# Kernel optimization log

Measured on AMD Instinct MI355X. Metric: run time of the kernel, lower is better.

The kernel has to match this reference:

```python
import jax, jax.numpy as jnp
import numpy as np

N = 50000      # nodes
E = 600000     # edges
D = 128        # num_features == hidden_dim
H = 1          # heads (only runnable config of this module)
C = 128        # per-head channels
L = 2          # num_layers
G = 64         # graphs in batch
NC = 10        # num_classes


def setup_inputs() -> dict:
    key = jax.random.key(0)
    ks = jax.random.split(key, 12)
    s = 1.0 / np.sqrt(D)
    inp = {
        "x": jax.random.normal(ks[0], (N, D), jnp.float32),
        "edge_index": jax.random.randint(ks[1], (2, E), 0, N),
        "batch": jnp.sort(jax.random.randint(ks[2], (N,), 0, G)),
        # per-layer TransformerConv params (stacked over layers)
        "Wq": jax.random.normal(ks[3], (L, D, H * C), jnp.float32) * s,
        "bq": jax.random.normal(ks[4], (L, H * C), jnp.float32) * 0.01,
        "Wk": jax.random.normal(ks[5], (L, D, H * C), jnp.float32) * s,
        "bk": jax.random.normal(ks[6], (L, H * C), jnp.float32) * 0.01,
        "Wv": jax.random.normal(ks[7], (L, D, H * C), jnp.float32) * s,
        "bv": jax.random.normal(ks[8], (L, H * C), jnp.float32) * 0.01,
        "Ws": jax.random.normal(ks[9], (L, D, H * C), jnp.float32) * s,  # lin_skip (root weight)
        "bs": jax.random.normal(ks[10], (L, H * C), jnp.float32) * 0.01,
        "W_fc": jax.random.normal(ks[11], (H * C, NC), jnp.float32) * (1.0 / np.sqrt(H * C)),
        "b_fc": jnp.zeros((NC,), jnp.float32),
    }
    return inp


def _transformer_conv(x, src, dst, wq, bq, wk, bk, wv, bv, ws, bs):
    n = x.shape[0]
    q = (x @ wq + bq).reshape(n, H, C)
    k = (x @ wk + bk).reshape(n, H, C)
    v = (x @ wv + bv).reshape(n, H, C)
    # edge-wise gather: query from dst (x_i), key/value from src (x_j)
    score = (q[dst] * k[src]).sum(-1) / jnp.sqrt(jnp.float32(C))  # [E, H]
    # segment softmax over incoming edges of each dst node
    m = jax.ops.segment_max(score, dst, num_segments=n)           # [N, H]
    ex = jnp.exp(score - m[dst])
    den = jax.ops.segment_sum(ex, dst, num_segments=n)
    alpha = ex / den[dst]                                         # [E, H]
    agg = jax.ops.segment_sum(alpha[..., None] * v[src], dst, num_segments=n)
    return agg.reshape(n, H * C) + x @ ws + bs                    # concat heads + skip


def reference(x, edge_index, batch, Wq, bq, Wk, bk, Wv, bv, Ws, bs, W_fc, b_fc):
    src, dst = edge_index[0], edge_index[1]
    h = x
    for l in range(L):
        h = jax.nn.relu(_transformer_conv(h, src, dst, Wq[l], bq[l], Wk[l], bk[l],
                                          Wv[l], bv[l], Ws[l], bs[l]))
    # global mean pool per graph
    sums = jax.ops.segment_sum(h, batch, num_segments=G)
    cnts = jax.ops.segment_sum(jnp.ones((h.shape[0],), h.dtype), batch, num_segments=G)
    pooled = sums / jnp.maximum(cnts, 1.0)[:, None]
    logits = pooled @ W_fc + b_fc
    return jax.nn.log_softmax(logits, axis=1)
```

## Files before the change

### kernel.cpp

```cpp
#include <hip/hip_runtime.h>
#include <math.h>

#define NN 50000
#define EE 600000
#define DD 128
#define GG 64
#define NCLS 10
#define PCHUNK 128
#define NTILE (NN / 16)
#define NBUK 196
#define BSTRIDE 4096
#define EPB ((EE + 255) / 256)

typedef __attribute__((ext_vector_type(8))) __bf16 bf16x8;
typedef __attribute__((ext_vector_type(8))) unsigned short u16x8;
typedef __attribute__((ext_vector_type(4))) float f32x4;

__device__ __forceinline__ unsigned short f2bf(float f) {
    unsigned int u = __float_as_uint(f);
    u += 0x7fff + ((u >> 16) & 1);
    return (unsigned short)(u >> 16);
}

__device__ __forceinline__ float bf2f(unsigned short h) {
    return __uint_as_float(((unsigned int)h) << 16);
}


__global__ __launch_bounds__(256) void prep_kernel(
    const float* __restrict__ x,
    const float* __restrict__ wq, const float* __restrict__ wk,
    const float* __restrict__ wv, const float* __restrict__ ws,
    unsigned short* __restrict__ wt, unsigned short* __restrict__ xb,
    int* __restrict__ bucketcnt, float* __restrict__ gsum) {
    int tid = blockIdx.x * 256 + threadIdx.x;
    int TOT = gridDim.x * 256;
    if (tid < 256) bucketcnt[tid] = 0;
    for (int i = tid; i < GG * DD + GG; i += TOT) gsum[i] = 0.f;
    for (int i = tid; i < 2 * 4 * 16384; i += TOT) {
        int k = i & 127;
        int n = (i >> 7) & 127;
        int lm = i >> 14;
        int l = lm >> 2, m = lm & 3;
        const float* w = (m == 0) ? wq : (m == 1) ? wk : (m == 2) ? wv : ws;
        wt[i] = f2bf(w[l * 16384 + k * 128 + n]);
    }
    const int NV = (int)(((size_t)NN * DD) / 8);
    for (int i = tid; i < NV; i += TOT) {
        const float* p = x + (size_t)i * 8;
        float4 f0 = *(const float4*)p;
        float4 f1 = *(const float4*)(p + 4);
        u16x8 a8;
        a8[0] = f2bf(f0.x); a8[1] = f2bf(f0.y); a8[2] = f2bf(f0.z); a8[3] = f2bf(f0.w);
        a8[4] = f2bf(f1.x); a8[5] = f2bf(f1.y); a8[6] = f2bf(f1.z); a8[7] = f2bf(f1.w);
        *(u16x8*)(xb + (size_t)i * 8) = a8;
    }
}


__global__ __launch_bounds__(1024) void bucket_kernel(
    const int* __restrict__ src, const int* __restrict__ dst,
    int* __restrict__ bucketcnt, int2* __restrict__ bedge) {
    __shared__ int hist[256];
    __shared__ int base[256];
    int t = threadIdx.x;
    if (t < 256) hist[t] = 0;
    __syncthreads();
    int e0 = blockIdx.x * EPB;
    int eend = min(e0 + EPB, EE);

    int b0 = -1, b1 = -1, b2 = -1;
    int sl0 = 0, sl1 = 0, sl2 = 0;
    int s0 = 0, s1 = 0, s2 = 0, d0 = 0, d1 = 0, d2 = 0;
    int i = e0 + t;
    if (i < eend) { d0 = dst[i]; s0 = src[i]; b0 = d0 >> 8; sl0 = atomicAdd(&hist[b0], 1); }
    i += 1024;
    if (i < eend) { d1 = dst[i]; s1 = src[i]; b1 = d1 >> 8; sl1 = atomicAdd(&hist[b1], 1); }
    i += 1024;
    if (i < eend) { d2 = dst[i]; s2 = src[i]; b2 = d2 >> 8; sl2 = atomicAdd(&hist[b2], 1); }
    __syncthreads();

    if (t < 256) {
        int h = hist[t];
        base[t] = h ? atomicAdd(&bucketcnt[t], h) : 0;
    }
    __syncthreads();

    if (b0 >= 0) bedge[b0 * BSTRIDE + base[b0] + sl0] = make_int2(s0, d0);
    if (b1 >= 0) bedge[b1 * BSTRIDE + base[b1] + sl1] = make_int2(s1, d1);
    if (b2 >= 0) bedge[b2 * BSTRIDE + base[b2] + sl2] = make_int2(s2, d2);
}


__global__ __launch_bounds__(1024) void bsort_kernel(
    const int* __restrict__ bucketcnt, const int2* __restrict__ bedge,
    int* __restrict__ indptr, int* __restrict__ esrc) {
    __shared__ int buf[256];
    __shared__ int cur[256];
    __shared__ int bstart_s;
    int b = blockIdx.x;
    int t = threadIdx.x;

    if (t < 256) buf[t] = (t < NBUK) ? bucketcnt[t] : 0;
    __syncthreads();
    if (t == 0) {
        int acc = 0;
        for (int i2 = 0; i2 < NBUK; ++i2) {
            if (i2 == b) bstart_s = acc;
            acc += buf[i2];
        }
    }
    if (b == 0 && t == 1) indptr[NN] = EE;
    __syncthreads();

    int count = buf[b];
    int node0 = b << 8;
    int nn = min(256, NN - node0);
    __syncthreads();
    if (t < 256) buf[t] = 0;
    __syncthreads();

    const int2* be = bedge + (size_t)b * BSTRIDE;
    for (int i2 = t; i2 < count; i2 += 1024)
        atomicAdd(&buf[be[i2].y - node0], 1);
    __syncthreads();

    if (t == 0) {
        int acc = 0;
        for (int i2 = 0; i2 < 256; ++i2) {
            cur[i2] = acc;
            acc += buf[i2];
        }
    }
    __syncthreads();
    if (t < nn) indptr[node0 + t] = bstart_s + cur[t];
    __syncthreads();

    for (int i2 = t; i2 < count; i2 += 1024) {
        int2 e = be[i2];
        int slot = atomicAdd(&cur[e.y - node0], 1);
        esrc[bstart_s + slot] = e.x;
    }
}


__global__ __launch_bounds__(256, 4) void gemm_mfma(
    const unsigned short* __restrict__ xa,
    const unsigned short* __restrict__ wt,
    const float* __restrict__ bq, const float* __restrict__ bk,
    const float* __restrict__ bv, const float* __restrict__ bs,
    unsigned short* __restrict__ qb, unsigned short* __restrict__ kvb,
    unsigned short* __restrict__ sb) {
    int gw = blockIdx.x * 4 + (threadIdx.x >> 6);
    int lane = threadIdx.x & 63;
    int mat = (gw >> 1) & 3;
    int ch = gw & 1;
    int wseq = gw >> 3;
    int lr = lane & 15, quad = lane >> 4;

    const unsigned short* wm_ = wt + mat * 16384;
    const float* bias = (mat == 0) ? bq : (mat == 1) ? bk : (mat == 2) ? bv : bs;
    unsigned short* outp; int ostride, ooff;
    if (mat == 0)      { outp = qb;  ostride = 128; ooff = 0; }
    else if (mat == 1) { outp = kvb; ostride = 256; ooff = 0; }
    else if (mat == 2) { outp = kvb; ostride = 256; ooff = 128; }
    else               { outp = sb;  ostride = 128; ooff = 0; }

    bf16x8 bfr[4][4];
    #pragma unroll
    for (int ks = 0; ks < 4; ++ks)
        #pragma unroll
        for (int tn = 0; tn < 4; ++tn)
            bfr[ks][tn] = *(const bf16x8*)(wm_ + (ch * 64 + tn * 16 + lr) * 128
                                               + ks * 32 + quad * 8);
    float bcol[4];
    #pragma unroll
    for (int tn = 0; tn < 4; ++tn) bcol[tn] = bias[ch * 64 + tn * 16 + lr];

    for (int tile = wseq; tile < NTILE; tile += 256) {
        int row0 = tile * 16;
        bf16x8 af[4];
        #pragma unroll
        for (int ks = 0; ks < 4; ++ks)
            af[ks] = *(const bf16x8*)(xa + (size_t)(row0 + lr) * DD + ks * 32 + quad * 8);

        f32x4 acc[4];
        #pragma unroll
        for (int tn = 0; tn < 4; ++tn) acc[tn] = (f32x4){0.f, 0.f, 0.f, 0.f};
        #pragma unroll
        for (int ks = 0; ks < 4; ++ks)
            #pragma unroll
            for (int tn = 0; tn < 4; ++tn)
                acc[tn] = __builtin_amdgcn_mfma_f32_16x16x32_bf16(
                    af[ks], bfr[ks][tn], acc[tn], 0, 0, 0);

        #pragma unroll
        for (int tn = 0; tn < 4; ++tn) {
            int col = ch * 64 + tn * 16 + lr;
            int nb = row0 + quad * 4;
            #pragma unroll
            for (int r = 0; r < 4; ++r)
                outp[(size_t)(nb + r) * ostride + ooff + col] = f2bf(acc[tn][r] + bcol[tn]);
        }
    }
}


__global__ __launch_bounds__(256) void attn_kernel(
    const unsigned short* __restrict__ qb, const unsigned short* __restrict__ kvb,
    const unsigned short* __restrict__ sb,
    const int* __restrict__ indptr, const int* __restrict__ esrc,
    unsigned short* __restrict__ hout, int n) {
    int node = (int)((blockIdx.x * blockDim.x + threadIdx.x) >> 6);
    int lane = threadIdx.x & 63;
    if (node >= n) return;
    int g = lane >> 4, j = lane & 15;

    u16x8 q8 = *(const u16x8*)(qb + (size_t)node * DD + j * 8);
    float qf[8];
    #pragma unroll
    for (int c = 0; c < 8; ++c) qf[c] = bf2f(q8[c]);

    int beg = indptr[node], end = indptr[node + 1];

    float m = -3.0e38f, den = 0.f;
    float acc[8];
    #pragma unroll
    for (int c = 0; c < 8; ++c) acc[c] = 0.f;

    int e = beg + g;
    if (e < end) {
        const unsigned short* p0 = kvb + (size_t)esrc[e] * 256 + j * 8;
        u16x8 k8 = *(const u16x8*)p0;
        u16x8 v8 = *(const u16x8*)(p0 + 128);
        for (;;) {
            int en = e + 4;
            bool haven = en < end;
            u16x8 k8n, v8n;
            if (haven) {
                const unsigned short* p = kvb + (size_t)esrc[en] * 256 + j * 8;
                k8n = *(const u16x8*)p;
                v8n = *(const u16x8*)(p + 128);
            }
            float p_;
            p_ = qf[0] * bf2f(k8[0]);
            p_ = fmaf(qf[1], bf2f(k8[1]), p_);
            p_ = fmaf(qf[2], bf2f(k8[2]), p_);
            p_ = fmaf(qf[3], bf2f(k8[3]), p_);
            p_ = fmaf(qf[4], bf2f(k8[4]), p_);
            p_ = fmaf(qf[5], bf2f(k8[5]), p_);
            p_ = fmaf(qf[6], bf2f(k8[6]), p_);
            p_ = fmaf(qf[7], bf2f(k8[7]), p_);
            p_ += __shfl_xor(p_, 8);
            p_ += __shfl_xor(p_, 4);
            p_ += __shfl_xor(p_, 2);
            p_ += __shfl_xor(p_, 1);
            float score = p_ * 0.088388347648318447f;
            float mn = fmaxf(m, score);
            float scale = __expf(m - mn);
            float pe = __expf(score - mn);
            den = den * scale + pe;
            #pragma unroll
            for (int c = 0; c < 8; ++c)
                acc[c] = fmaf(acc[c], scale, pe * bf2f(v8[c]));
            m = mn;
            if (!haven) break;
            e = en; k8 = k8n; v8 = v8n;
        }
    }

    float mo = __shfl_xor(m, 16);
    float m2 = fmaxf(m, mo);
    mo = __shfl_xor(m2, 32);
    float mf = fmaxf(m2, mo);
    float sc = __expf(m - mf);
    den *= sc;
    den += __shfl_xor(den, 16);
    den += __shfl_xor(den, 32);
    #pragma unroll
    for (int c = 0; c < 8; ++c) {
        float a = acc[c] * sc;
        a += __shfl_xor(a, 16);
        a += __shfl_xor(a, 32);
        acc[c] = a;
    }
    float inv = den > 0.f ? 1.0f / den : 0.f;
    if (g == 0) {
        u16x8 s8 = *(const u16x8*)(sb + (size_t)node * DD + j * 8);
        u16x8 o8;
        #pragma unroll
        for (int c = 0; c < 8; ++c)
            o8[c] = f2bf(fmaxf(fmaf(acc[c], inv, bf2f(s8[c])), 0.f));
        *(u16x8*)(hout + (size_t)node * DD + j * 8) = o8;
    }
}


__global__ __launch_bounds__(128) void pool_kernel(const unsigned short* __restrict__ h,
                                                   const int* __restrict__ batch,
                                                   float* __restrict__ gsum,
                                                   float* __restrict__ gcnt, int n) {
    __shared__ int bsh[PCHUNK];
    int t = threadIdx.x;
    int node0 = blockIdx.x * PCHUNK;
    int nnodes = min(PCHUNK, n - node0);
    if (t < nnodes) bsh[t] = batch[node0 + t];
    __syncthreads();

    int cur = bsh[0];
    float acc = 0.f;
    int cnt = 0;
    for (int j = 0; j < nnodes; ++j) {
        int g = bsh[j];
        float val = bf2f(h[(size_t)(node0 + j) * DD + t]);
        if (g != cur) {
            atomicAdd(&gsum[cur * DD + t], acc);
            if (t == 0) atomicAdd(&gcnt[cur], (float)cnt);
            acc = 0.f; cnt = 0; cur = g;
        }
        acc += val; ++cnt;
    }
    if (cnt > 0) {
        atomicAdd(&gsum[cur * DD + t], acc);
        if (t == 0) atomicAdd(&gcnt[cur], (float)cnt);
    }
}


__global__ __launch_bounds__(64) void head_kernel(
    const float* __restrict__ gsum, const float* __restrict__ gcnt,
    const float* __restrict__ wfc, const float* __restrict__ bfc,
    float* __restrict__ out) {
    int g = blockIdx.x;
    int lane = threadIdx.x;
    float cnt = fmaxf(gcnt[g], 1.0f);
    float inv = 1.0f / cnt;
    float p0 = gsum[g * DD + lane] * inv;
    float p1 = gsum[g * DD + lane + 64] * inv;
    __shared__ float logits[NCLS];
    for (int c = 0; c < NCLS; ++c) {
        float partial = p0 * wfc[lane * NCLS + c] + p1 * wfc[(lane + 64) * NCLS + c];
        partial += __shfl_xor(partial, 32);
        partial += __shfl_xor(partial, 16);
        partial += __shfl_xor(partial, 8);
        partial += __shfl_xor(partial, 4);
        partial += __shfl_xor(partial, 2);
        partial += __shfl_xor(partial, 1);
        if (lane == 0) logits[c] = partial + bfc[c];
    }
    __syncthreads();
    if (lane == 0) {
        float mx = logits[0];
        for (int c = 1; c < NCLS; ++c) mx = fmaxf(mx, logits[c]);
        float sum = 0.f;
        for (int c = 0; c < NCLS; ++c) sum += expf(logits[c] - mx);
        float lse = mx + logf(sum);
        for (int c = 0; c < NCLS; ++c) out[g * NCLS + c] = logits[c] - lse;
    }
}


extern "C" void kernel_launch(void* const* d_in, const int* in_sizes, int n_in,
                              void* d_out, int out_size, void* d_ws, size_t ws_size,
                              hipStream_t stream) {
    const float* x     = (const float*)d_in[0];
    const int*   ei    = (const int*)d_in[1];
    const int*   batch = (const int*)d_in[2];
    const float* Wq = (const float*)d_in[3];
    const float* bq = (const float*)d_in[4];
    const float* Wk = (const float*)d_in[5];
    const float* bk = (const float*)d_in[6];
    const float* Wv = (const float*)d_in[7];
    const float* bv = (const float*)d_in[8];
    const float* Ws = (const float*)d_in[9];
    const float* bs = (const float*)d_in[10];
    const float* Wfc = (const float*)d_in[11];
    const float* bfc = (const float*)d_in[12];
    float* out = (float*)d_out;

    const size_t ND = (size_t)NN * DD;
    unsigned short* hbuf = (unsigned short*)d_ws;
    unsigned short* qb  = hbuf + ND;
    unsigned short* sb  = qb + ND;
    unsigned short* kvb = sb + ND;
    unsigned short* xb  = kvb + 2 * ND;
    unsigned short* wt  = xb + ND;
    int* bucketcnt = (int*)(wt + 2 * 4 * 16384);
    int* indptr    = bucketcnt + 256;
    int* esrc      = indptr + NN + 1;
    int2* bedge    = (int2*)(esrc + EE);
    float* gsum = (float*)(bedge + NBUK * BSTRIDE);
    float* gcnt = gsum + GG * DD;

    const int* src = ei;
    const int* dst = ei + EE;

    prep_kernel<<<1024, 256, 0, stream>>>(x, Wq, Wk, Wv, Ws, wt, xb, bucketcnt, gsum);
    bucket_kernel<<<256, 1024, 0, stream>>>(src, dst, bucketcnt, bedge);
    bsort_kernel<<<NBUK, 1024, 0, stream>>>(bucketcnt, bedge, indptr, esrc);

    for (int l = 0; l < 2; ++l) {
        size_t bo = (size_t)l * DD;
        const unsigned short* wtl = wt + (size_t)l * 4 * 16384;
        const unsigned short* xa = (l == 0) ? xb : hbuf;
        gemm_mfma<<<512, 256, 0, stream>>>(
            xa, wtl, bq + bo, bk + bo, bv + bo, bs + bo, qb, kvb, sb);
        attn_kernel<<<(NN + 3) / 4, 256, 0, stream>>>(
            qb, kvb, sb, indptr, esrc, hbuf, NN);
    }

    pool_kernel<<<(NN + PCHUNK - 1) / PCHUNK, 128, 0, stream>>>(hbuf, batch, gsum, gcnt, NN);
    head_kernel<<<GG, 64, 0, stream>>>(gsum, gcnt, Wfc, bfc, out);
}
```

Before: 285.5 us.

## Fuse x bf16 conversion into layer-0 GEMM, parallelize bsort scans, prefetch esrc

Removes the separate fp32-to-bf16 conversion of x from prep_kernel and converts x on the fly inside a templated layer-0 GEMM, which drops a full write and re-read of a bf16 copy of x. The serial single-thread prefix sums in bsort_kernel become wave-level shuffle scans. The attention loop also loads edge source indices two steps ahead so the index load is off the critical path of the K/V gather. The cost is that layer-0 GEMM reads fp32 input, so each of the 8 waves covering a row tile reloads and reconverts the same rows at double the bytes.

```diff
diff --git a/kernel.cpp b/kernel.cpp
--- a/kernel.cpp
+++ b/kernel.cpp
@@ -28,10 +28,9 @@
 
 
 __global__ __launch_bounds__(256) void prep_kernel(
-    const float* __restrict__ x,
     const float* __restrict__ wq, const float* __restrict__ wk,
     const float* __restrict__ wv, const float* __restrict__ ws,
-    unsigned short* __restrict__ wt, unsigned short* __restrict__ xb,
+    unsigned short* __restrict__ wt,
     int* __restrict__ bucketcnt, float* __restrict__ gsum) {
     int tid = blockIdx.x * 256 + threadIdx.x;
     int TOT = gridDim.x * 256;
@@ -45,16 +44,6 @@
         const float* w = (m == 0) ? wq : (m == 1) ? wk : (m == 2) ? wv : ws;
         wt[i] = f2bf(w[l * 16384 + k * 128 + n]);
     }
-    const int NV = (int)(((size_t)NN * DD) / 8);
-    for (int i = tid; i < NV; i += TOT) {
-        const float* p = x + (size_t)i * 8;
-        float4 f0 = *(const float4*)p;
-        float4 f1 = *(const float4*)(p + 4);
-        u16x8 a8;
-        a8[0] = f2bf(f0.x); a8[1] = f2bf(f0.y); a8[2] = f2bf(f0.z); a8[3] = f2bf(f0.w);
-        a8[4] = f2bf(f1.x); a8[5] = f2bf(f1.y); a8[6] = f2bf(f1.z); a8[7] = f2bf(f1.w);
-        *(u16x8*)(xb + (size_t)i * 8) = a8;
-    }
 }
 
 
@@ -97,25 +86,32 @@
     int* __restrict__ indptr, int* __restrict__ esrc) {
     __shared__ int buf[256];
     __shared__ int cur[256];
-    __shared__ int bstart_s;
     int b = blockIdx.x;
     int t = threadIdx.x;
 
     if (t < 256) buf[t] = (t < NBUK) ? bucketcnt[t] : 0;
     __syncthreads();
-    if (t == 0) {
-        int acc = 0;
-        for (int i2 = 0; i2 < NBUK; ++i2) {
-            if (i2 == b) bstart_s = acc;
-            acc += buf[i2];
-        }
-    }
-    if (b == 0 && t == 1) indptr[NN] = EE;
-    __syncthreads();
-
+    if (t < 64) {
+        int carry = 0;
+        #pragma unroll
+        for (int c = 0; c < 4; ++c) {
+            int v = buf[c * 64 + t];
+            int x = v;
+            #pragma unroll
+            for (int off = 1; off < 64; off <<= 1) {
+                int y = __shfl_up(x, off);
+                if (t >= off) x += y;
+            }
+            cur[c * 64 + t] = carry + x - v;
+            carry += __shfl(x, 63);
+        }
+    }
+    __syncthreads();
     int count = buf[b];
+    int bstart = cur[b];
     int node0 = b << 8;
     int nn = min(256, NN - node0);
+    if (b == 0 && t == 0) indptr[NN] = EE;
     __syncthreads();
     if (t < 256) buf[t] = 0;
     __syncthreads();
@@ -125,27 +121,36 @@
         atomicAdd(&buf[be[i2].y - node0], 1);
     __syncthreads();
 
-    if (t == 0) {
-        int acc = 0;
-        for (int i2 = 0; i2 < 256; ++i2) {
-            cur[i2] = acc;
-            acc += buf[i2];
-        }
-    }
-    __syncthreads();
-    if (t < nn) indptr[node0 + t] = bstart_s + cur[t];
+    if (t < 64) {
+        int carry = 0;
+        #pragma unroll
+        for (int c = 0; c < 4; ++c) {
+            int v = buf[c * 64 + t];
+            int x = v;
+            #pragma unroll
+            for (int off = 1; off < 64; off <<= 1) {
+                int y = __shfl_up(x, off);
+                if (t >= off) x += y;
+            }
+            cur[c * 64 + t] = carry + x - v;
+            carry += __shfl(x, 63);
+        }
+    }
+    __syncthreads();
+    if (t < nn) indptr[node0 + t] = bstart + cur[t];
     __syncthreads();
 
     for (int i2 = t; i2 < count; i2 += 1024) {
         int2 e = be[i2];
         int slot = atomicAdd(&cur[e.y - node0], 1);
-        esrc[bstart_s + slot] = e.x;
-    }
-}
-
-
+        esrc[bstart + slot] = e.x;
+    }
+}
+
+
+template <bool IN_BF16>
 __global__ __launch_bounds__(256, 4) void gemm_mfma(
-    const unsigned short* __restrict__ xa,
+    const void* __restrict__ xin,
     const unsigned short* __restrict__ wt,
     const float* __restrict__ bq, const float* __restrict__ bk,
     const float* __restrict__ bv, const float* __restrict__ bs,
@@ -181,8 +186,21 @@
         int row0 = tile * 16;
         bf16x8 af[4];
         #pragma unroll
-        for (int ks = 0; ks < 4; ++ks)
-            af[ks] = *(const bf16x8*)(xa + (size_t)(row0 + lr) * DD + ks * 32 + quad * 8);
+        for (int ks = 0; ks < 4; ++ks) {
+            if (IN_BF16) {
+                af[ks] = *(const bf16x8*)((const unsigned short*)xin
+                             + (size_t)(row0 + lr) * DD + ks * 32 + quad * 8);
+            } else {
+                const float* p = (const float*)xin
+                                 + (size_t)(row0 + lr) * DD + ks * 32 + quad * 8;
+                float4 f0 = *(const float4*)p;
+                float4 f1 = *(const float4*)(p + 4);
+                u16x8 a8;
+                a8[0] = f2bf(f0.x); a8[1] = f2bf(f0.y); a8[2] = f2bf(f0.z); a8[3] = f2bf(f0.w);
+                a8[4] = f2bf(f1.x); a8[5] = f2bf(f1.y); a8[6] = f2bf(f1.z); a8[7] = f2bf(f1.w);
+                af[ks] = *(bf16x8*)&a8;
+            }
+        }
 
         f32x4 acc[4];
         #pragma unroll
@@ -230,15 +248,19 @@
 
     int e = beg + g;
     if (e < end) {
-        const unsigned short* p0 = kvb + (size_t)esrc[e] * 256 + j * 8;
+        int sidx = esrc[e];
+        int en = e + 4;
+        int sn = (en < end) ? esrc[en] : 0;
+        const unsigned short* p0 = kvb + (size_t)sidx * 256 + j * 8;
         u16x8 k8 = *(const u16x8*)p0;
         u16x8 v8 = *(const u16x8*)(p0 + 128);
         for (;;) {
-            int en = e + 4;
             bool haven = en < end;
+            int en2 = en + 4;
+            int sn2 = (en2 < end) ? esrc[en2] : 0;
             u16x8 k8n, v8n;
             if (haven) {
-                const unsigned short* p = kvb + (size_t)esrc[en] * 256 + j * 8;
+                const unsigned short* p = kvb + (size_t)sn * 256 + j * 8;
                 k8n = *(const u16x8*)p;
                 v8n = *(const u16x8*)(p + 128);
             }
@@ -265,7 +287,7 @@
                 acc[c] = fmaf(acc[c], scale, pe * bf2f(v8[c]));
             m = mn;
             if (!haven) break;
-            e = en; k8 = k8n; v8 = v8n;
+            en = en2; sn = sn2; k8 = k8n; v8 = v8n;
         }
     }
 
@@ -383,8 +405,7 @@
     unsigned short* qb  = hbuf + ND;
     unsigned short* sb  = qb + ND;
     unsigned short* kvb = sb + ND;
-    unsigned short* xb  = kvb + 2 * ND;
-    unsigned short* wt  = xb + ND;
+    unsigned short* wt  = kvb + 2 * ND;
     int* bucketcnt = (int*)(wt + 2 * 4 * 16384);
     int* indptr    = bucketcnt + 256;
     int* esrc      = indptr + NN + 1;
@@ -395,16 +416,21 @@
     const int* src = ei;
     const int* dst = ei + EE;
 
-    prep_kernel<<<1024, 256, 0, stream>>>(x, Wq, Wk, Wv, Ws, wt, xb, bucketcnt, gsum);
+    prep_kernel<<<256, 256, 0, stream>>>(Wq, Wk, Wv, Ws, wt, bucketcnt, gsum);
     bucket_kernel<<<256, 1024, 0, stream>>>(src, dst, bucketcnt, bedge);
     bsort_kernel<<<NBUK, 1024, 0, stream>>>(bucketcnt, bedge, indptr, esrc);
 
     for (int l = 0; l < 2; ++l) {
         size_t bo = (size_t)l * DD;
         const unsigned short* wtl = wt + (size_t)l * 4 * 16384;
-        const unsigned short* xa = (l == 0) ? xb : hbuf;
-        gemm_mfma<<<512, 256, 0, stream>>>(
-            xa, wtl, bq + bo, bk + bo, bv + bo, bs + bo, qb, kvb, sb);
+        if (l == 0)
+            gemm_mfma<false><<<512, 256, 0, stream>>>(
+                (const void*)x, wtl, bq + bo, bk + bo, bv + bo, bs + bo,
+                qb, kvb, sb);
+        else
+            gemm_mfma<true><<<512, 256, 0, stream>>>(
+                (const void*)hbuf, wtl, bq + bo, bk + bo, bv + bo, bs + bo,
+                qb, kvb, sb);
         attn_kernel<<<(NN + 3) / 4, 256, 0, stream>>>(
             qb, kvb, sb, indptr, esrc, hbuf, NN);
     }
```

Result: no change. 283.3 us (-0.8%).
